# Kernel optimization log

Measured on AMD Instinct MI355X. Metric: run time of the kernel, lower is better.

Reference implementation:

```python
import jax, jax.numpy as jnp
import numpy as np

V, E, H, OUT = 100000, 300, 256, 3
B, LS, LT = 128, 128, 8


def _lstm_scan(xs, Wih, Whh, bih, bhh, reverse):
    # xs: [T, B, E] time-major; returns hidden states [T, B, H] in original time order
    h0 = jnp.zeros((xs.shape[1], H), xs.dtype)
    def step(carry, x):
        h, c = carry
        g = x @ Wih.T + bih + h @ Whh.T + bhh  # [B, 4H]
        i, f, gg, o = jnp.split(g, 4, axis=-1)
        c = jax.nn.sigmoid(f) * c + jax.nn.sigmoid(i) * jnp.tanh(gg)
        h = jax.nn.sigmoid(o) * jnp.tanh(c)
        return (h, c), h
    _, hs = jax.lax.scan(step, (h0, h0), xs, reverse=reverse)
    return hs


def _bidir(emb_bte, Wih_f, Whh_f, bih_f, bhh_f, Wih_b, Whh_b, bih_b, bhh_b):
    xs = jnp.transpose(emb_bte, (1, 0, 2))  # [T, B, E]
    hf = _lstm_scan(xs, Wih_f, Whh_f, bih_f, bhh_f, False)
    hb = _lstm_scan(xs, Wih_b, Whh_b, bih_b, bhh_b, True)
    return jnp.transpose(jnp.concatenate([hf, hb], axis=-1), (1, 0, 2))  # [B, T, 2H]


def setup_inputs() -> dict:
    key = jax.random.key(0)
    ks = jax.random.split(key, 32)
    n = lambda i, shape: 0.05 * jax.random.normal(ks[i], shape, dtype=jnp.float32)
    inp = {
        "sentence_source": jax.random.randint(ks[0], (B, LS), 0, V),
        "target_source": jax.random.randint(ks[1], (B, LT), 0, V),
        "emb_W": n(2, (V, E)),
    }
    names = ["sf", "sb", "tf", "tb"]
    for j, nm in enumerate(names):
        base = 3 + 4 * j
        inp[f"Wih_{nm}"] = n(base + 0, (4 * H, E))
        inp[f"Whh_{nm}"] = n(base + 1, (4 * H, H))
        inp[f"bih_{nm}"] = n(base + 2, (4 * H,))
        inp[f"bhh_{nm}"] = n(base + 3, (4 * H,))
    inp["Wout"] = n(20, (OUT, 2 * H))
    inp["bout"] = n(21, (OUT,))
    return inp


def reference(sentence_source, target_source, emb_W,
              Wih_sf, Whh_sf, bih_sf, bhh_sf,
              Wih_sb, Whh_sb, bih_sb, bhh_sb,
              Wih_tf, Whh_tf, bih_tf, bhh_tf,
              Wih_tb, Whh_tb, bih_tb, bhh_tb,
              Wout, bout):
    emb = emb_W.at[0].set(0.0)  # padding_idx=0
    sen = emb[sentence_source]  # [B, LS, E]  (dropout is identity at eval)
    tgt = emb[target_source]    # [B, LT, E]
    sen_h = _bidir(sen, Wih_sf, Whh_sf, bih_sf, bhh_sf, Wih_sb, Whh_sb, bih_sb, bhh_sb)  # [B, LS, 2H]
    tgt_h = _bidir(tgt, Wih_tf, Whh_tf, bih_tf, bhh_tf, Wih_tb, Whh_tb, bih_tb, bhh_tb)  # [B, LT, 2H]
    A = jnp.einsum("bsh,bth->bst", sen_h, tgt_h)          # [B, LS, LT]
    col = jax.nn.softmax(A, axis=1)
    row = jax.nn.softmax(A, axis=2)
    row_vec = jnp.mean(row, axis=1, keepdims=True)         # [B, 1, LT]
    attn = jnp.einsum("bst,bqt->bsq", col, row_vec)        # [B, LS, 1]
    score = jnp.einsum("bsq,bsh->bqh", attn, sen_h)        # [B, 1, 2H]
    logits = score @ Wout.T + bout                         # [B, 1, OUT]
    return jax.nn.softmax(logits, axis=-1).squeeze()       # [B, OUT]
```

## Files before the change

kernel.cpp:

```cpp
#include <hip/hip_runtime.h>


typedef unsigned short u16;
typedef unsigned long long u64;
typedef float f32x4 __attribute__((ext_vector_type(4)));
typedef int   i32x4 __attribute__((ext_vector_type(4)));
typedef short bf16x8 __attribute__((ext_vector_type(8)));
typedef short s16x4 __attribute__((ext_vector_type(4)));
typedef unsigned short u16x4 __attribute__((ext_vector_type(4)));

#define KP 320
#define KPL 328
#define FH 1024
#define HH 256

struct Ptr4 { const float* p[4]; };

static __device__ __forceinline__ u16 f2bf(float f) {
    unsigned int u = __float_as_uint(f);
    u += 0x7FFFu + ((u >> 16) & 1u);
    return (u16)(u >> 16);
}
static __device__ __forceinline__ float bf2f(u16 s) {
    return __uint_as_float((unsigned int)s << 16);
}
static __device__ __forceinline__ float sigm(float x) {
    return __builtin_amdgcn_rcpf(1.0f + __expf(-x));
}
static __device__ __forceinline__ float tanh_(float x) {
    return 1.0f - 2.0f * __builtin_amdgcn_rcpf(1.0f + __expf(2.0f * x));
}

__global__ void embed_kernel(const int* __restrict__ sen, const int* __restrict__ tgt,
                             const float* __restrict__ emb,
                             u16* __restrict__ Xs, u16* __restrict__ Xt)
{
    int row = blockIdx.x;
    int tok; u16* dst;
    if (row < 16384) { tok = sen[row]; dst = Xs + (size_t)row * KP; }
    else             { tok = tgt[row - 16384]; dst = Xt + (size_t)(row - 16384) * KP; }
    const float* src = emb + (size_t)tok * 300;
    for (int k = threadIdx.x; k < KP; k += blockDim.x) {
        float v = (k < 300 && tok != 0) ? src[k] : 0.0f;
        dst[k] = f2bf(v);
    }
}

__global__ __launch_bounds__(256) void prep_weights_kernel(
    Ptr4 Wih, Ptr4 bih, Ptr4 bhh, u16* __restrict__ WihB, float* __restrict__ biasB)
{
    int dir = blockIdx.y;
    int idx = blockIdx.x * 256 + threadIdx.x;
    if (idx < FH * KP) {
        int row = idx / KP, k = idx - row * KP;
        WihB[(size_t)dir * FH * KP + idx] = (k < 300) ? f2bf(Wih.p[dir][row * 300 + k]) : (u16)0;
    }
    if (idx < FH) biasB[dir * FH + idx] = bih.p[dir][idx] + bhh.p[dir][idx];
}

__global__ __launch_bounds__(64) void whh_quant_kernel(
    Ptr4 Whh, char* __restrict__ Wq, float* __restrict__ wdq)
{
    int dir = blockIdx.y, row = blockIdx.x, tid = threadIdx.x;
    const float* src = Whh.p[dir] + (size_t)row * HH;
    float m = 0.0f;
    for (int k = tid; k < HH; k += 64) m = fmaxf(m, fabsf(src[k]));
    for (int off = 32; off; off >>= 1) m = fmaxf(m, __shfl_down(m, off));
    m = __shfl(m, 0);
    float qs = (m > 0.0f) ? 127.0f / m : 0.0f;
    char* dst = Wq + (size_t)dir * FH * HH + (size_t)row * HH;
    for (int k = tid; k < HH; k += 64) dst[k] = (char)(int)rintf(src[k] * qs);
    if (tid == 0) wdq[dir * FH + row] = (m > 0.0f) ? m / (127.0f * 127.0f) : 0.0f;
}

__global__ __launch_bounds__(256) void input_gemm_kernel(
    const u16* __restrict__ X, const u16* __restrict__ W,
    const float* __restrict__ bias, u16* __restrict__ G, size_t dirStride)
{
    __shared__ u16 Bs[64][KPL];

    int nwg = gridDim.x;
    int cpx = nwg >> 3;
    int wid = ((int)blockIdx.x & 7) * cpx + ((int)blockIdx.x >> 3);
    int nblk = wid & 31;
    int mblk = wid >> 5;
    int dirb = nblk >> 4;
    int u0   = (nblk & 15) * 16;

    int tid = threadIdx.x;
    int wave = tid >> 6, lane = tid & 63;
    int r = lane & 15, quad = lane >> 4;
    int m0 = mblk * 64 + wave * 16;

#pragma unroll
    for (int it = 0; it < 10; ++it) {
        int idx = it * 256 + tid;
        int row = idx / 40, cc = idx - row * 40;
        int j = row >> 4, rr = row & 15;
        bf16x8 v = *(const bf16x8*)(W + ((size_t)dirb * FH + j * 256 + u0 + rr) * KP + cc * 8);
        *(bf16x8*)&Bs[row][cc * 8] = v;
    }
    __syncthreads();

    const u16* xr = X + (size_t)(m0 + r) * KP + quad * 8;
    f32x4 acc[4] = {};
#pragma unroll
    for (int k0 = 0; k0 < KP; k0 += 32) {
        bf16x8 a = *(const bf16x8*)(xr + k0);
#pragma unroll
        for (int j = 0; j < 4; ++j) {
            bf16x8 b = *(const bf16x8*)&Bs[j * 16 + r][k0 + quad * 8];
            acc[j] = __builtin_amdgcn_mfma_f32_16x16x32_bf16(a, b, acc[j], 0, 0, 0);
        }
    }

#pragma unroll
    for (int reg = 0; reg < 4; ++reg) {
        int m = m0 + quad * 4 + reg;
        int unit = u0 + r;
        u16x4 ov;
#pragma unroll
        for (int j = 0; j < 4; ++j)
            ov[j] = f2bf(acc[j][reg] + bias[dirb * FH + j * 256 + unit]);
        *(u16x4*)(G + (size_t)dirb * dirStride + (size_t)m * FH + unit * 4) = ov;
    }
}

__global__ __launch_bounds__(1024, 1) void lstm_scan_kernel(
    const char*  __restrict__ WqB,
    const float* __restrict__ wdq,
    const u16*   __restrict__ Gs,
    const u16*   __restrict__ Gt,
    float* __restrict__ senH,
    float* __restrict__ tgtH)
{
    const int bx  = blockIdx.x;
    const int dir = bx >> 3;
    const int b0  = (bx & 7) << 4;
    const int T   = (dir < 2) ? 128 : 8;
    const int rev = dir & 1;

    const char* Wq = WqB + (size_t)dir * FH * HH;
    const u16*  G  = (dir < 2) ? (Gs + (size_t)dir * 16384 * FH)
                               : (Gt + (size_t)(dir - 2) * 1024 * FH);
    float* Hout = (dir < 2) ? senH : tgtH;
    const int hofs = rev ? 256 : 0;

    const int tid  = threadIdx.x;
    const int w    = tid >> 6, lane = tid & 63;
    const int r    = lane & 15, quad = lane >> 4;
    const int u    = w * 16 + r;

    __shared__ char hb8[2][16][272];

    u64 Bq[4][8];
    float dqv[4];
#pragma unroll
    for (int g = 0; g < 4; ++g) {
        int row = g * 256 + u;
        dqv[g] = wdq[dir * FH + row];
#pragma unroll
        for (int kt = 0; kt < 8; ++kt)
            Bq[g][kt] = *(const u64*)(Wq + ((size_t)row << 8) + kt * 32 + quad * 8);
    }

    for (int i = tid; i < 2 * 16 * 272; i += 1024) (&hb8[0][0][0])[i] = 0;
    __syncthreads();

    float c[4] = {};
    float hreg[4] = {};
    int tprev = 0;

    s16x4 gvA[4], gvB[4];
    {
        const int t0 = rev ? (T - 1) : 0;
#pragma unroll
        for (int reg = 0; reg < 4; ++reg)
            gvA[reg] = *(const s16x4*)(G + ((size_t)(b0 + quad * 4 + reg) * T + t0) * FH
                                       + u * 4);
    }

    auto body = [&](int cur, s16x4 (&gvU)[4], s16x4 (&gvP)[4],
                    int t, int tn, int doStore) {
#pragma unroll
        for (int reg = 0; reg < 4; ++reg)
            gvP[reg] = *(const s16x4*)(G + ((size_t)(b0 + quad * 4 + reg) * T + tn) * FH
                                       + u * 4);
        if (doStore) {
#pragma unroll
            for (int reg = 0; reg < 4; ++reg)
                Hout[((size_t)(b0 + quad * 4 + reg) * T + tprev) * 512 + hofs + u]
                    = hreg[reg];
        }

        i32x4 acc[4] = {};
#pragma unroll
        for (int kt = 0; kt < 8; ++kt) {
            u64 a = *(const u64*)&hb8[cur][r][quad * 8 + kt * 32];
#pragma unroll
            for (int g = 0; g < 4; ++g)
                acc[g] = __builtin_amdgcn_mfma_i32_16x16x32_i8(
                    (long long)a, (long long)Bq[g][kt], acc[g], 0, 0, 0);
        }

#pragma unroll
        for (int reg = 0; reg < 4; ++reg) {
            int bb = quad * 4 + reg;
            float pi = (float)acc[0][reg] * dqv[0] + bf2f((u16)gvU[reg].x);
            float pf = (float)acc[1][reg] * dqv[1] + bf2f((u16)gvU[reg].y);
            float pg = (float)acc[2][reg] * dqv[2] + bf2f((u16)gvU[reg].z);
            float po = (float)acc[3][reg] * dqv[3] + bf2f((u16)gvU[reg].w);
            float ig = sigm(pi), fg = sigm(pf), gg = tanh_(pg), og = sigm(po);
            float cn = fg * c[reg] + ig * gg;
            c[reg] = cn;
            float hn = og * tanh_(cn);
            hb8[cur ^ 1][bb][u] = (char)(int)rintf(hn * 127.0f);
            hreg[reg] = hn;
        }
        tprev = t;
        __syncthreads();
    };

    for (int s2 = 0; s2 < T; s2 += 2) {
        const int tA = rev ? (T - 1 - s2) : s2;
        const int tB = rev ? (T - 2 - s2) : (s2 + 1);
        const int tC = (s2 + 2 < T) ? (rev ? (T - 3 - s2) : (s2 + 2)) : tB;
        body(0, gvA, gvB, tA, tB, s2 > 0);
        body(1, gvB, gvA, tB, tC, 1);
    }

#pragma unroll
    for (int reg = 0; reg < 4; ++reg)
        Hout[((size_t)(b0 + quad * 4 + reg) * T + tprev) * 512 + hofs + u] = hreg[reg];
}

__global__ __launch_bounds__(256) void attn_out_kernel(
    const float* __restrict__ senH, const float* __restrict__ tgtH,
    const float* __restrict__ Wout, const float* __restrict__ bout,
    float* __restrict__ out)
{
    int b = blockIdx.x, tid = threadIdx.x;
    __shared__ float tg[8][512];
    __shared__ float Am[128][9];
    __shared__ float rowm[128][9];
    __shared__ float mcol[8], csum[8], rvec[8], attn[128], score[512], lg[3];

    const float* tgg = tgtH + (size_t)b * 8 * 512;
    for (int i = tid; i < 4096; i += 256) tg[i >> 9][i & 511] = tgg[i];
    __syncthreads();

    {
        int s = tid >> 1, t0 = (tid & 1) * 4;
        const float* sr = senH + ((size_t)b * 128 + s) * 512;
        float d0 = 0, d1 = 0, d2 = 0, d3 = 0;
        for (int h = 0; h < 512; ++h) {
            float x = sr[h];
            d0 += x * tg[t0 + 0][h]; d1 += x * tg[t0 + 1][h];
            d2 += x * tg[t0 + 2][h]; d3 += x * tg[t0 + 3][h];
        }
        Am[s][t0 + 0] = d0; Am[s][t0 + 1] = d1; Am[s][t0 + 2] = d2; Am[s][t0 + 3] = d3;
    }
    __syncthreads();

    if (tid < 8) {
        float m = -1e30f;
        for (int s = 0; s < 128; ++s) m = fmaxf(m, Am[s][tid]);
        float sum = 0;
        for (int s = 0; s < 128; ++s) sum += __expf(Am[s][tid] - m);
        mcol[tid] = m; csum[tid] = sum;
    }
    if (tid >= 64 && tid < 192) {
        int s = tid - 64;
        float m = -1e30f;
        for (int t = 0; t < 8; ++t) m = fmaxf(m, Am[s][t]);
        float e[8], sum = 0;
        for (int t = 0; t < 8; ++t) { e[t] = __expf(Am[s][t] - m); sum += e[t]; }
        float inv = __builtin_amdgcn_rcpf(sum);
        for (int t = 0; t < 8; ++t) rowm[s][t] = e[t] * inv;
    }
    __syncthreads();
    if (tid < 8) {
        float sum = 0;
        for (int s = 0; s < 128; ++s) sum += rowm[s][tid];
        rvec[tid] = sum * (1.0f / 128.0f);
    }
    __syncthreads();
    if (tid < 128) {
        float a = 0;
        for (int t = 0; t < 8; ++t)
            a += __expf(Am[tid][t] - mcol[t]) / csum[t] * rvec[t];
        attn[tid] = a;
    }
    __syncthreads();
    for (int h = tid; h < 512; h += 256) {
        float acc = 0;
        const float* sp = senH + (size_t)b * 128 * 512 + h;
        for (int s = 0; s < 128; ++s) acc += attn[s] * sp[(size_t)s * 512];
        score[h] = acc;
    }
    __syncthreads();
    if (tid < 3) {
        float acc = bout[tid];
        const float* wr = Wout + tid * 512;
        for (int h = 0; h < 512; ++h) acc += score[h] * wr[h];
        lg[tid] = acc;
    }
    __syncthreads();
    if (tid == 0) {
        float m = fmaxf(lg[0], fmaxf(lg[1], lg[2]));
        float e0 = __expf(lg[0] - m), e1 = __expf(lg[1] - m), e2 = __expf(lg[2] - m);
        float inv = 1.0f / (e0 + e1 + e2);
        out[b * 3 + 0] = e0 * inv; out[b * 3 + 1] = e1 * inv; out[b * 3 + 2] = e2 * inv;
    }
}

extern "C" void kernel_launch(void* const* d_in, const int* in_sizes, int n_in,
                              void* d_out, int out_size, void* d_ws, size_t ws_size,
                              hipStream_t stream)
{
    const int*   sen = (const int*)d_in[0];
    const int*   tgt = (const int*)d_in[1];
    const float* emb = (const float*)d_in[2];
    Ptr4 Wih = {{(const float*)d_in[3],  (const float*)d_in[7],
                 (const float*)d_in[11], (const float*)d_in[15]}};
    Ptr4 Whh = {{(const float*)d_in[4],  (const float*)d_in[8],
                 (const float*)d_in[12], (const float*)d_in[16]}};
    Ptr4 bih = {{(const float*)d_in[5],  (const float*)d_in[9],
                 (const float*)d_in[13], (const float*)d_in[17]}};
    Ptr4 bhh = {{(const float*)d_in[6],  (const float*)d_in[10],
                 (const float*)d_in[14], (const float*)d_in[18]}};
    const float* Wout = (const float*)d_in[19];
    const float* bout = (const float*)d_in[20];
    float* out = (float*)d_out;

    char* ws = (char*)d_ws;
    size_t off = 0;
    auto alloc = [&](size_t bytes) -> void* {
        void* p = ws + off; off += (bytes + 255) & ~(size_t)255; return p;
    };
    u16*   Xs    = (u16*)alloc((size_t)16384 * KP * 2);
    u16*   Xt    = (u16*)alloc((size_t)1024 * KP * 2);
    u16*   WihB  = (u16*)alloc((size_t)4 * FH * KP * 2);
    char*  WqB   = (char*)alloc((size_t)4 * FH * HH);
    float* wdq   = (float*)alloc((size_t)4 * FH * 4);
    float* biasB = (float*)alloc((size_t)4 * FH * 4);
    u16*   Gs    = (u16*)alloc((size_t)2 * 16384 * FH * 2);
    u16*   Gt    = (u16*)alloc((size_t)2 * 1024 * FH * 2);
    float* senH  = (float*)alloc((size_t)128 * 128 * 512 * 4);
    float* tgtH  = (float*)alloc((size_t)128 * 8 * 512 * 4);
    (void)ws_size; (void)in_sizes; (void)n_in; (void)out_size;

    embed_kernel<<<17408, 128, 0, stream>>>(sen, tgt, emb, Xs, Xt);
    prep_weights_kernel<<<dim3(1280, 4), 256, 0, stream>>>(Wih, bih, bhh, WihB, biasB);
    whh_quant_kernel<<<dim3(FH, 4), 64, 0, stream>>>(Whh, WqB, wdq);

    input_gemm_kernel<<<8192, 256, 0, stream>>>(Xs, WihB, biasB, Gs,
                                                (size_t)16384 * FH);
    input_gemm_kernel<<<512, 256, 0, stream>>>(Xt, WihB + (size_t)2 * FH * KP,
                                               biasB + 2 * FH, Gt,
                                               (size_t)1024 * FH);

    lstm_scan_kernel<<<32, 1024, 0, stream>>>(WqB, wdq, Gs, Gt, senH, tgtH);
    attn_out_kernel<<<128, 256, 0, stream>>>(senH, tgtH, Wout, bout, out);
}
```

Before: 601.3 us.

## Merge prep kernels, fold log2e into weights, use 16x16x64 int8 MFMA

Merges the embedding, Wih conversion and Whh quantisation kernels into one launch, and the two input GEMM launches into one, cutting launch overhead. It pre-scales the gate weights, biases and dequant factors by log2(e) (2·log2(e) for the g gate) so the recurrence can call exp2 directly. The scan uses the wider 16x16x64 int8 MFMA with 16-byte loads, halving the MFMA count per step. The gate tensor G is laid out time-major so each step's loads are contiguous. The cost is more index math, and the cell-state tanh still uses the old exp path.

```diff
diff --git a/kernel.cpp b/kernel.cpp
--- a/kernel.cpp
+++ b/kernel.cpp
@@ -13,6 +13,7 @@
 #define KPL 328
 #define FH 1024
 #define HH 256
+#define L2E 1.4426950408889634f
 
 struct Ptr4 { const float* p[4]; };
 
@@ -24,68 +25,90 @@
 static __device__ __forceinline__ float bf2f(u16 s) {
     return __uint_as_float((unsigned int)s << 16);
 }
-static __device__ __forceinline__ float sigm(float x) {
-    return __builtin_amdgcn_rcpf(1.0f + __expf(-x));
+static __device__ __forceinline__ float sigm2(float x) {
+    return __builtin_amdgcn_rcpf(1.0f + __builtin_amdgcn_exp2f(-x));
+}
+static __device__ __forceinline__ float tanh2(float x) {
+    return 1.0f - 2.0f * __builtin_amdgcn_rcpf(1.0f + __builtin_amdgcn_exp2f(x));
 }
 static __device__ __forceinline__ float tanh_(float x) {
     return 1.0f - 2.0f * __builtin_amdgcn_rcpf(1.0f + __expf(2.0f * x));
 }
 
-__global__ void embed_kernel(const int* __restrict__ sen, const int* __restrict__ tgt,
-                             const float* __restrict__ emb,
-                             u16* __restrict__ Xs, u16* __restrict__ Xt)
-{
-    int row = blockIdx.x;
-    int tok; u16* dst;
-    if (row < 16384) { tok = sen[row]; dst = Xs + (size_t)row * KP; }
-    else             { tok = tgt[row - 16384]; dst = Xt + (size_t)(row - 16384) * KP; }
-    const float* src = emb + (size_t)tok * 300;
-    for (int k = threadIdx.x; k < KP; k += blockDim.x) {
-        float v = (k < 300 && tok != 0) ? src[k] : 0.0f;
-        dst[k] = f2bf(v);
-    }
-}
-
-__global__ __launch_bounds__(256) void prep_weights_kernel(
-    Ptr4 Wih, Ptr4 bih, Ptr4 bhh, u16* __restrict__ WihB, float* __restrict__ biasB)
-{
-    int dir = blockIdx.y;
-    int idx = blockIdx.x * 256 + threadIdx.x;
-    if (idx < FH * KP) {
-        int row = idx / KP, k = idx - row * KP;
-        WihB[(size_t)dir * FH * KP + idx] = (k < 300) ? f2bf(Wih.p[dir][row * 300 + k]) : (u16)0;
-    }
-    if (idx < FH) biasB[dir * FH + idx] = bih.p[dir][idx] + bhh.p[dir][idx];
-}
-
-__global__ __launch_bounds__(64) void whh_quant_kernel(
-    Ptr4 Whh, char* __restrict__ Wq, float* __restrict__ wdq)
-{
-    int dir = blockIdx.y, row = blockIdx.x, tid = threadIdx.x;
-    const float* src = Whh.p[dir] + (size_t)row * HH;
-    float m = 0.0f;
-    for (int k = tid; k < HH; k += 64) m = fmaxf(m, fabsf(src[k]));
-    for (int off = 32; off; off >>= 1) m = fmaxf(m, __shfl_down(m, off));
-    m = __shfl(m, 0);
-    float qs = (m > 0.0f) ? 127.0f / m : 0.0f;
-    char* dst = Wq + (size_t)dir * FH * HH + (size_t)row * HH;
-    for (int k = tid; k < HH; k += 64) dst[k] = (char)(int)rintf(src[k] * qs);
-    if (tid == 0) wdq[dir * FH + row] = (m > 0.0f) ? m / (127.0f * 127.0f) : 0.0f;
+__global__ __launch_bounds__(256) void pre_kernel(
+    const int* __restrict__ sen, const int* __restrict__ tgt,
+    const float* __restrict__ emb, Ptr4 Wih, Ptr4 Whh, Ptr4 bih, Ptr4 bhh,
+    u16* __restrict__ Xs, u16* __restrict__ Xt,
+    u16* __restrict__ WihB, float* __restrict__ biasB,
+    char* __restrict__ Wq, float* __restrict__ wdq)
+{
+    int bid = blockIdx.x, tid = threadIdx.x;
+    if (bid < 17408) {
+        int row = bid;
+        int tok; u16* dst;
+        if (row < 16384) { tok = sen[row]; dst = Xs + (size_t)row * KP; }
+        else             { tok = tgt[row - 16384]; dst = Xt + (size_t)(row - 16384) * KP; }
+        const float* src = emb + (size_t)tok * 300;
+        for (int k = tid; k < KP; k += 256) {
+            float v = (k < 300 && tok != 0) ? src[k] : 0.0f;
+            dst[k] = f2bf(v);
+        }
+    } else if (bid < 22528) {
+        int local = bid - 17408;
+        int dir = local / 1280, blk = local - dir * 1280;
+        int idx = blk * 256 + tid;
+        if (idx < FH * KP) {
+            int row = idx / KP, k = idx - row * KP;
+            float gsc = ((row >> 8) == 2) ? 2.0f * L2E : L2E;
+            WihB[(size_t)dir * FH * KP + idx] =
+                (k < 300) ? f2bf(Wih.p[dir][row * 300 + k] * gsc) : (u16)0;
+        }
+        if (idx < FH) {
+            float gsc = ((idx >> 8) == 2) ? 2.0f * L2E : L2E;
+            biasB[dir * FH + idx] = (bih.p[dir][idx] + bhh.p[dir][idx]) * gsc;
+        }
+    } else {
+        int local = bid - 22528;
+        int w = tid >> 6, lane = tid & 63;
+        int pair = local * 4 + w;
+        int dir = pair >> 10, row = pair & 1023;
+        const float* src = Whh.p[dir] + (size_t)row * HH;
+        float m = 0.0f;
+        for (int k = lane; k < HH; k += 64) m = fmaxf(m, fabsf(src[k]));
+        for (int off = 32; off; off >>= 1) m = fmaxf(m, __shfl_down(m, off));
+        m = __shfl(m, 0);
+        float qs = (m > 0.0f) ? 127.0f / m : 0.0f;
+        char* dst = Wq + (size_t)dir * FH * HH + (size_t)row * HH;
+        for (int k = lane; k < HH; k += 64) dst[k] = (char)(int)rintf(src[k] * qs);
+        if (lane == 0) {
+            float gsc = ((row >> 8) == 2) ? 2.0f * L2E : L2E;
+            wdq[dir * FH + row] = (m > 0.0f) ? m / (127.0f * 127.0f) * gsc : 0.0f;
+        }
+    }
 }
 
 __global__ __launch_bounds__(256) void input_gemm_kernel(
-    const u16* __restrict__ X, const u16* __restrict__ W,
-    const float* __restrict__ bias, u16* __restrict__ G, size_t dirStride)
+    const u16* __restrict__ Xs, const u16* __restrict__ Xt,
+    const u16* __restrict__ WihB, const float* __restrict__ biasB,
+    u16* __restrict__ Gs, u16* __restrict__ Gt)
 {
     __shared__ u16 Bs[64][KPL];
 
-    int nwg = gridDim.x;
+    int bid = blockIdx.x;
+    const u16* X; const u16* W; const float* bias; u16* G;
+    int lbid, nwg, tsh;
+    if (bid < 8192) { lbid = bid;        nwg = 8192; tsh = 7;
+                      X = Xs; W = WihB;                         bias = biasB;          G = Gs; }
+    else            { lbid = bid - 8192; nwg = 512;  tsh = 3;
+                      X = Xt; W = WihB + (size_t)2 * FH * KP;   bias = biasB + 2 * FH; G = Gt; }
+
     int cpx = nwg >> 3;
-    int wid = ((int)blockIdx.x & 7) * cpx + ((int)blockIdx.x >> 3);
+    int wid = (lbid & 7) * cpx + (lbid >> 3);
     int nblk = wid & 31;
     int mblk = wid >> 5;
     int dirb = nblk >> 4;
     int u0   = (nblk & 15) * 16;
+    size_t dirStride = (size_t)(tsh == 7 ? 16384 : 1024) * FH;
 
     int tid = threadIdx.x;
     int wave = tid >> 6, lane = tid & 63;
@@ -117,12 +140,13 @@
 #pragma unroll
     for (int reg = 0; reg < 4; ++reg) {
         int m = m0 + quad * 4 + reg;
+        int b = m >> tsh, t = m & ((1 << tsh) - 1);
         int unit = u0 + r;
         u16x4 ov;
 #pragma unroll
         for (int j = 0; j < 4; ++j)
             ov[j] = f2bf(acc[j][reg] + bias[dirb * FH + j * 256 + unit]);
-        *(u16x4*)(G + (size_t)dirb * dirStride + (size_t)m * FH + unit * 4) = ov;
+        *(u16x4*)(G + (size_t)dirb * dirStride + ((size_t)t * 128 + b) * FH + unit * 4) = ov;
     }
 }
 
@@ -151,17 +175,17 @@
     const int r    = lane & 15, quad = lane >> 4;
     const int u    = w * 16 + r;
 
-    __shared__ char hb8[2][16][272];
-
-    u64 Bq[4][8];
+    __shared__ __align__(16) char hb8[2][16][272];
+
+    i32x4 Bq[4][4];
     float dqv[4];
 #pragma unroll
     for (int g = 0; g < 4; ++g) {
         int row = g * 256 + u;
         dqv[g] = wdq[dir * FH + row];
 #pragma unroll
-        for (int kt = 0; kt < 8; ++kt)
-            Bq[g][kt] = *(const u64*)(Wq + ((size_t)row << 8) + kt * 32 + quad * 8);
+        for (int kt = 0; kt < 4; ++kt)
+            Bq[g][kt] = *(const i32x4*)(Wq + ((size_t)row << 8) + kt * 64 + quad * 16);
     }
 
     for (int i = tid; i < 2 * 16 * 272; i += 1024) (&hb8[0][0][0])[i] = 0;
@@ -176,7 +200,7 @@
         const int t0 = rev ? (T - 1) : 0;
 #pragma unroll
         for (int reg = 0; reg < 4; ++reg)
-            gvA[reg] = *(const s16x4*)(G + ((size_t)(b0 + quad * 4 + reg) * T + t0) * FH
+            gvA[reg] = *(const s16x4*)(G + ((size_t)t0 * 128 + b0 + quad * 4 + reg) * FH
                                        + u * 4);
     }
 
@@ -184,7 +208,7 @@
                     int t, int tn, int doStore) {
 #pragma unroll
         for (int reg = 0; reg < 4; ++reg)
-            gvP[reg] = *(const s16x4*)(G + ((size_t)(b0 + quad * 4 + reg) * T + tn) * FH
+            gvP[reg] = *(const s16x4*)(G + ((size_t)tn * 128 + b0 + quad * 4 + reg) * FH
                                        + u * 4);
         if (doStore) {
 #pragma unroll
@@ -195,12 +219,11 @@
 
         i32x4 acc[4] = {};
 #pragma unroll
-        for (int kt = 0; kt < 8; ++kt) {
-            u64 a = *(const u64*)&hb8[cur][r][quad * 8 + kt * 32];
+        for (int kt = 0; kt < 4; ++kt) {
+            i32x4 a = *(const i32x4*)&hb8[cur][r][kt * 64 + quad * 16];
 #pragma unroll
             for (int g = 0; g < 4; ++g)
-                acc[g] = __builtin_amdgcn_mfma_i32_16x16x32_i8(
-                    (long long)a, (long long)Bq[g][kt], acc[g], 0, 0, 0);
+                acc[g] = __builtin_amdgcn_mfma_i32_16x16x64_i8(a, Bq[g][kt], acc[g], 0, 0, 0);
         }
 
 #pragma unroll
@@ -210,7 +233,7 @@
             float pf = (float)acc[1][reg] * dqv[1] + bf2f((u16)gvU[reg].y);
             float pg = (float)acc[2][reg] * dqv[2] + bf2f((u16)gvU[reg].z);
             float po = (float)acc[3][reg] * dqv[3] + bf2f((u16)gvU[reg].w);
-            float ig = sigm(pi), fg = sigm(pf), gg = tanh_(pg), og = sigm(po);
+            float ig = sigm2(pi), fg = sigm2(pf), gg = tanh2(pg), og = sigm2(po);
             float cn = fg * c[reg] + ig * gg;
             c[reg] = cn;
             float hn = og * tanh_(cn);
@@ -350,16 +373,9 @@
     float* tgtH  = (float*)alloc((size_t)128 * 8 * 512 * 4);
     (void)ws_size; (void)in_sizes; (void)n_in; (void)out_size;
 
-    embed_kernel<<<17408, 128, 0, stream>>>(sen, tgt, emb, Xs, Xt);
-    prep_weights_kernel<<<dim3(1280, 4), 256, 0, stream>>>(Wih, bih, bhh, WihB, biasB);
-    whh_quant_kernel<<<dim3(FH, 4), 64, 0, stream>>>(Whh, WqB, wdq);
-
-    input_gemm_kernel<<<8192, 256, 0, stream>>>(Xs, WihB, biasB, Gs,
-                                                (size_t)16384 * FH);
-    input_gemm_kernel<<<512, 256, 0, stream>>>(Xt, WihB + (size_t)2 * FH * KP,
-                                               biasB + 2 * FH, Gt,
-                                               (size_t)1024 * FH);
-
+    pre_kernel<<<23552, 256, 0, stream>>>(sen, tgt, emb, Wih, Whh, bih, bhh,
+                                          Xs, Xt, WihB, biasB, WqB, wdq);
+    input_gemm_kernel<<<8704, 256, 0, stream>>>(Xs, Xt, WihB, biasB, Gs, Gt);
     lstm_scan_kernel<<<32, 1024, 0, stream>>>(WqB, wdq, Gs, Gt, senH, tgtH);
     attn_out_kernel<<<128, 256, 0, stream>>>(senH, tgtH, Wout, bout, out);
 }
```

After: 577.4 us. 4.0% less time.
